# Performance work log

Hardware: AMD Instinct MI355X
Metric: run time of the kernel (lower is better)

The kernel has to match this reference:

```python
import jax, jax.numpy as jnp
import numpy as np

B, N, C, H, W = 2, 6, 64, 28, 50
D = 59  # len(arange(1.0, 60.0, 1.0))
BH, BW = 200, 200
BEV_X0, BEV_Y0 = -50.0, -50.0
RES_X, RES_Y = 0.5, 0.5  # (50-(-50))/200


def setup_inputs() -> dict:
    key = jax.random.key(0)
    k1, k2 = jax.random.split(key)
    features = jax.random.normal(k1, (B, N, C, H, W), dtype=jnp.float32)
    # depth distribution over D bins (softmax-normalized, as a depth net would emit)
    depth = jax.nn.softmax(jax.random.normal(k2, (B, N, D, H, W), dtype=jnp.float32), axis=2)
    # realistic pinhole intrinsics for a WxH feature map
    K = np.zeros((B, N, 3, 3), np.float32)
    K[..., 0, 0] = float(W)
    K[..., 1, 1] = float(W)
    K[..., 0, 2] = W / 2.0
    K[..., 1, 2] = H / 2.0
    K[..., 2, 2] = 1.0
    # cam-to-ego extrinsics: axis remap (z_cam->x_ego, x_cam->-y_ego, y_cam->-z_ego)
    # composed with a per-camera yaw, plus a small mounting translation
    R0 = np.array([[0, 0, 1], [-1, 0, 0], [0, -1, 0]], np.float32)
    E = np.zeros((B, N, 4, 4), np.float32)
    for n in range(N):
        yaw = 2.0 * np.pi * n / N
        Rz = np.array([[np.cos(yaw), -np.sin(yaw), 0.0],
                       [np.sin(yaw), np.cos(yaw), 0.0],
                       [0.0, 0.0, 1.0]], np.float32)
        E[:, n, :3, :3] = Rz @ R0
        E[:, n, 0, 3] = 1.5 * np.cos(yaw)
        E[:, n, 1, 3] = 1.5 * np.sin(yaw)
        E[:, n, 2, 3] = 1.6
    E[..., 3, 3] = 1.0
    return {
        "features": features,
        "depth": depth,
        "intrinsics": jnp.asarray(K),
        "extrinsics": jnp.asarray(E),
    }


def _frustum_ego(intrinsics, extrinsics):
    # pixel grid (H, W, 3) homogeneous coords
    xs = jnp.linspace(0.0, W - 1.0, W, dtype=jnp.float32)
    ys = jnp.linspace(0.0, H - 1.0, H, dtype=jnp.float32)
    yy, xx = jnp.meshgrid(ys, xs, indexing="ij")
    pix = jnp.stack([xx, yy, jnp.ones_like(xx)], axis=-1)  # (H, W, 3)
    depth_bins = jnp.arange(1.0, 60.0, 1.0, dtype=jnp.float32)  # (D,)
    frustum_cam = pix[None] * depth_bins[:, None, None, None]  # (D, H, W, 3)
    K_inv = jnp.linalg.inv(intrinsics)  # (B, N, 3, 3)
    cam = jnp.einsum("bnij,dhwj->bndhwi", K_inv, frustum_cam)  # (B, N, D, H, W, 3)
    R = extrinsics[..., :3, :3]
    t = extrinsics[..., :3, 3]
    ego = jnp.einsum("bnij,bndhwj->bndhwi", R, cam) + t[:, :, None, None, None, :]
    return ego


def reference(features, depth, intrinsics, extrinsics):
    ego = _frustum_ego(intrinsics, extrinsics)  # (B, N, D, H, W, 3)

    # lift: outer product of features (B,N,C,H,W) and depth (B,N,D,H,W)
    lifted = features[:, :, None] * depth[:, :, :, None]  # (B, N, D, C, H, W)
    lifted = lifted.transpose(0, 1, 2, 4, 5, 3).reshape(B, -1, C)  # b (n d h w) c

    fr = ego.reshape(B, -1, 3)  # b (n d h w) xyz
    x, y, z = fr[..., 0], fr[..., 1], fr[..., 2]
    # torch .long() truncates toward zero -> astype(int32) matches
    bx = ((x - BEV_X0) / RES_X).astype(jnp.int32)
    by = ((y - BEV_Y0) / RES_Y).astype(jnp.int32)
    valid = (bx >= 0) & (bx < BW) & (by >= 0) & (by < BH) & (z > 0)

    # flat scatter index with per-batch offset; invalid -> dummy segment (dropped)
    b_off = (jnp.arange(B, dtype=jnp.int32) * (BH * BW))[:, None]
    flat_idx = jnp.where(valid, b_off + by * BW + bx, B * BH * BW)
    seg = jax.ops.segment_sum(
        lifted.reshape(-1, C), flat_idx.reshape(-1), num_segments=B * BH * BW + 1
    )
    bev = seg[: B * BH * BW].reshape(B, BH, BW, C).transpose(0, 3, 1, 2)  # (B, C, BH, BW)
    return bev
```

## Files before the change

kernel.cpp:

```cpp
#include <hip/hip_runtime.h>
#include <hip/hip_bf16.h>

#define Bc 2
#define Nc 6
#define Cc 64
#define Hc 28
#define Wc 50
#define Dc 59
#define BHc 200
#define BWc 200

#define DSPLIT 2
#define DCHUNK 32
#define DWAVE 8

__global__ __launch_bounds__(256) void fp_scatter3(
    const float* __restrict__ feats,
    const float* __restrict__ depth,
    const float* __restrict__ Kmat,
    const float* __restrict__ Emat,
    float* __restrict__ acc)
{
    __shared__ __align__(16) float feat_lds[Hc][Cc];
    __shared__ __align__(16) float mdep[Hc][DCHUNK];

    int blk   = blockIdx.x;
    int dhalf = blk & 1;
    int pix   = blk >> 1;
    int w  = pix % Wc;
    int bn = pix / Wc;
    int b  = bn / Nc;
    int tid  = threadIdx.x;
    int lane = tid & 63;
    int wid  = tid >> 6;

    const size_t HW = (size_t)Hc * Wc;
    const float* fbase = feats + (size_t)bn * Cc * HW + w;
    const float* dbase = depth + (size_t)bn * Dc * HW + w;

    for (int h = wid; h < Hc; h += 4)
        feat_lds[h][lane] = fbase[(size_t)lane * HW + (size_t)h * Wc];

    const float* K = Kmat + (size_t)bn * 9;
    float k00 = K[0], k01 = K[1], k02 = K[2];
    float k10 = K[3], k11 = K[4], k12 = K[5];
    float k20 = K[6], k21 = K[7], k22 = K[8];

    float c00 = __fsub_rn(__fmul_rn(k11, k22), __fmul_rn(k12, k21));
    float c01 = __fsub_rn(__fmul_rn(k12, k20), __fmul_rn(k10, k22));
    float c02 = __fsub_rn(__fmul_rn(k10, k21), __fmul_rn(k11, k20));
    float det = __fadd_rn(__fadd_rn(__fmul_rn(k00, c00), __fmul_rn(k01, c01)),
                          __fmul_rn(k02, c02));
    float i00 = __fdiv_rn(c00, det);
    float i01 = __fdiv_rn(__fsub_rn(__fmul_rn(k02, k21), __fmul_rn(k01, k22)), det);
    float i02 = __fdiv_rn(__fsub_rn(__fmul_rn(k01, k12), __fmul_rn(k02, k11)), det);
    float i10 = __fdiv_rn(c01, det);
    float i11 = __fdiv_rn(__fsub_rn(__fmul_rn(k00, k22), __fmul_rn(k02, k20)), det);
    float i12 = __fdiv_rn(__fsub_rn(__fmul_rn(k02, k10), __fmul_rn(k00, k12)), det);
    float i20 = __fdiv_rn(c02, det);
    float i21 = __fdiv_rn(__fsub_rn(__fmul_rn(k01, k20), __fmul_rn(k00, k21)), det);
    float i22 = __fdiv_rn(__fsub_rn(__fmul_rn(k00, k11), __fmul_rn(k01, k10)), det);

    const float* E = Emat + (size_t)bn * 16;
    float r00 = E[0], r01 = E[1], r02 = E[2],  tx = E[3];
    float r10 = E[4], r11 = E[5], r12 = E[6],  ty = E[7];
    float r20 = E[8], r21 = E[9], r22 = E[10], tz = E[11];

    __syncthreads();

    float* accb = acc + (size_t)b * (BHc * BWc) * Cc;

    int h = lane;
    float xf = (float)w;
    float yf = (float)h;
    int ld0 = wid * DWAVE;

    float accv[DWAVE];
    int   prim[DWAVE];

#pragma unroll
    for (int k = 0; k < DWAVE; ++k) {
        accv[k] = 0.0f;
        prim[k] = -1;
        int ld = ld0 + k;
        int dg = dhalf * DCHUNK + ld;
        if (dg < Dc) {
            float db = (float)(dg + 1);
            float dep = 0.0f;
            if (h < Hc) dep = dbase[(size_t)dg * HW + (size_t)h * Wc];

            float px = __fmul_rn(xf, db);
            float py = __fmul_rn(yf, db);
            float pz = db;

            float cx = __fadd_rn(__fadd_rn(__fmul_rn(i00, px), __fmul_rn(i01, py)), __fmul_rn(i02, pz));
            float cy = __fadd_rn(__fadd_rn(__fmul_rn(i10, px), __fmul_rn(i11, py)), __fmul_rn(i12, pz));
            float cz = __fadd_rn(__fadd_rn(__fmul_rn(i20, px), __fmul_rn(i21, py)), __fmul_rn(i22, pz));

            float ex = __fadd_rn(__fadd_rn(__fadd_rn(__fmul_rn(r00, cx), __fmul_rn(r01, cy)), __fmul_rn(r02, cz)), tx);
            float ey = __fadd_rn(__fadd_rn(__fadd_rn(__fmul_rn(r10, cx), __fmul_rn(r11, cy)), __fmul_rn(r12, cz)), ty);
            float ez = __fadd_rn(__fadd_rn(__fadd_rn(__fmul_rn(r20, cx), __fmul_rn(r21, cy)), __fmul_rn(r22, cz)), tz);

            int bx = (int)(__fmul_rn(__fadd_rn(ex, 50.0f), 2.0f));
            int by = (int)(__fmul_rn(__fadd_rn(ey, 50.0f), 2.0f));

            bool valid = (h < Hc) & (bx >= 0) & (bx < BWc) & (by >= 0) & (by < BHc) & (ez > 0.0f);
            int binidx = by * BWc + bx;

            unsigned long long vm = __ballot(valid);
            float val = 0.0f;
            if (vm != 0ULL) {
                int first = __builtin_ctzll(vm);
                int pr = __shfl(binidx, first);
                unsigned long long match = __ballot(valid && (binidx == pr));
                unsigned long long rest  = vm & ~match;
                prim[k] = pr;
                val = (valid && (binidx == pr)) ? dep : 0.0f;

                while (rest) {
                    int hh2 = __builtin_ctzll(rest);
                    rest &= rest - 1;
                    int   bidx = __shfl(binidx, hh2);
                    float dv   = __shfl(dep, hh2);
                    atomicAdd(&accb[(size_t)bidx * Cc + lane],
                              __fmul_rn(feat_lds[hh2][lane], dv));
                }
            }
            if (h < Hc) {
                char* base = (char*)&mdep[h][0];
                *(float*)(base + (((ld << 2) ^ ((h & 7) << 4)))) = val;
            }
        }
    }

    int lb0 = ld0 >> 2;
#pragma unroll
    for (int hh = 0; hh < Hc; ++hh) {
        float f = feat_lds[hh][lane];
        const float4* rowp = (const float4*)&mdep[hh][0];
        float4 v0 = rowp[(lb0 + 0) ^ (hh & 7)];
        float4 v1 = rowp[(lb0 + 1) ^ (hh & 7)];
        accv[0] = __builtin_fmaf(f, v0.x, accv[0]);
        accv[1] = __builtin_fmaf(f, v0.y, accv[1]);
        accv[2] = __builtin_fmaf(f, v0.z, accv[2]);
        accv[3] = __builtin_fmaf(f, v0.w, accv[3]);
        accv[4] = __builtin_fmaf(f, v1.x, accv[4]);
        accv[5] = __builtin_fmaf(f, v1.y, accv[5]);
        accv[6] = __builtin_fmaf(f, v1.z, accv[6]);
        accv[7] = __builtin_fmaf(f, v1.w, accv[7]);
    }

#pragma unroll
    for (int k = 0; k < DWAVE; ++k) {
        if (prim[k] >= 0)
            atomicAdd(&accb[(size_t)prim[k] * Cc + lane], accv[k]);
    }
}

__global__ __launch_bounds__(256) void fp_transpose_kernel(
    const float* __restrict__ acc, float* __restrict__ out)
{
    __shared__ float tile[64][65];
    const int P = BHc * BWc;
    int b = blockIdx.y;
    int p0 = blockIdx.x * 64;
    int tx = threadIdx.x & 63;
    int ty = threadIdx.x >> 6;

    const float* src = acc + (size_t)b * P * Cc;
#pragma unroll
    for (int i = 0; i < 16; ++i) {
        int row = ty * 16 + i;
        tile[row][tx] = src[(size_t)(p0 + row) * Cc + tx];
    }
    __syncthreads();
    float* dst = out + (size_t)b * Cc * P;
#pragma unroll
    for (int i = 0; i < 16; ++i) {
        int c = ty * 16 + i;
        dst[(size_t)c * P + p0 + tx] = tile[tx][c];
    }
}

extern "C" void kernel_launch(void* const* d_in, const int* in_sizes, int n_in,
                              void* d_out, int out_size, void* d_ws, size_t ws_size,
                              hipStream_t stream) {
    const float* feats = (const float*)d_in[0];
    const float* depth = (const float*)d_in[1];
    const float* Kmat  = (const float*)d_in[2];
    const float* Emat  = (const float*)d_in[3];
    float* out = (float*)d_out;

    const size_t ACC_ELEMS = (size_t)Bc * BHc * BWc * Cc;
    const size_t ACC_BYTES = ACC_ELEMS * sizeof(float);
    float* acc = (float*)d_ws;

    hipMemsetAsync(acc, 0, ACC_BYTES, stream);

    const int NBLK = Bc * Nc * Wc * DSPLIT;
    fp_scatter3<<<NBLK, 256, 0, stream>>>(feats, depth, Kmat, Emat, acc);

    fp_transpose_kernel<<<dim3((BHc * BWc) / 64, Bc), 256, 0, stream>>>(acc, out);
}
```

Measured before the change: 118.6 us.

## Pre-transpose features and depth for coalesced loads, split depth into four chunks

Adds a pre-pass kernel that transposes features to (bn,h,w,c) and depth to (bn,d,w,h) in workspace, so the scatter kernel reads them with contiguous, coalesced loads instead of strided ones. The scatter kernel now splits the depth range into four chunks of 16 (four bins per wave), which doubles the block count and shrinks the per-thread accumulator arrays. The cost is an extra kernel launch and a full extra read and write of both inputs, plus features being reloaded by twice as many blocks.

```diff
diff --git a/kernel.cpp b/kernel.cpp
--- a/kernel.cpp
+++ b/kernel.cpp
@@ -10,23 +10,75 @@
 #define BHc 200
 #define BWc 200
 
-#define DSPLIT 2
-#define DCHUNK 32
-#define DWAVE 8
-
-__global__ __launch_bounds__(256) void fp_scatter3(
+#define DSPLIT 4
+#define DCHUNK 16
+#define DWAVE 4
+
+#define HWc (Hc * Wc)
+#define NT1 (Bc * Nc * 22)
+#define NT2 (Bc * Nc * Dc)
+
+__global__ __launch_bounds__(256) void fp_pretrans(
     const float* __restrict__ feats,
     const float* __restrict__ depth,
+    float* __restrict__ Fp,
+    float* __restrict__ Dpp)
+{
+    __shared__ float t[64][65];
+    __shared__ float t2[Hc][Wc + 1];
+
+    int bid = blockIdx.x;
+    int tid = threadIdx.x;
+
+    if (bid < NT1) {
+        int bn  = bid / 22;
+        int hw0 = (bid % 22) * 64;
+        int tx = tid & 63;
+        int ty = tid >> 6;
+        const float* src = feats + (size_t)bn * Cc * HWc;
+        float* dst = Fp + (size_t)bn * HWc * Cc;
+#pragma unroll
+        for (int i = 0; i < 16; ++i) {
+            int c = ty * 16 + i;
+            int hw = hw0 + tx;
+            t[c][tx] = (hw < HWc) ? src[(size_t)c * HWc + hw] : 0.0f;
+        }
+        __syncthreads();
+#pragma unroll
+        for (int i = 0; i < 16; ++i) {
+            int j = ty * 16 + i;
+            if (hw0 + j < HWc)
+                dst[(size_t)(hw0 + j) * Cc + tx] = t[tx][j];
+        }
+    } else {
+        int bid2 = bid - NT1;
+        int bn = bid2 / Dc;
+        int d  = bid2 % Dc;
+        const float* sp = depth + ((size_t)bn * Dc + d) * HWc;
+        float* dp = Dpp + ((size_t)bn * Dc + d) * HWc;
+        for (int idx = tid; idx < HWc; idx += 256)
+            t2[idx / Wc][idx % Wc] = sp[idx];
+        __syncthreads();
+        for (int idx = tid; idx < HWc; idx += 256) {
+            int w = idx / Hc, h = idx % Hc;
+            dp[idx] = t2[h][w];
+        }
+    }
+}
+
+__global__ __launch_bounds__(256) void fp_scatter4(
+    const float* __restrict__ Fp,
+    const float* __restrict__ Dpp,
     const float* __restrict__ Kmat,
     const float* __restrict__ Emat,
     float* __restrict__ acc)
 {
     __shared__ __align__(16) float feat_lds[Hc][Cc];
-    __shared__ __align__(16) float mdep[Hc][DCHUNK];
-
-    int blk   = blockIdx.x;
-    int dhalf = blk & 1;
-    int pix   = blk >> 1;
+    __shared__ __align__(16) float mdep[Hc][20];
+
+    int bid = blockIdx.x;
+    int dq  = bid & (DSPLIT - 1);
+    int pix = bid >> 2;
     int w  = pix % Wc;
     int bn = pix / Wc;
     int b  = bn / Nc;
@@ -34,12 +86,9 @@
     int lane = tid & 63;
     int wid  = tid >> 6;
 
-    const size_t HW = (size_t)Hc * Wc;
-    const float* fbase = feats + (size_t)bn * Cc * HW + w;
-    const float* dbase = depth + (size_t)bn * Dc * HW + w;
-
-    for (int h = wid; h < Hc; h += 4)
-        feat_lds[h][lane] = fbase[(size_t)lane * HW + (size_t)h * Wc];
+    const float* fbase = Fp + ((size_t)bn * Hc * Wc + w) * Cc;
+    for (int hh = wid; hh < Hc; hh += 4)
+        feat_lds[hh][lane] = fbase[(size_t)hh * Wc * Cc + lane];
 
     const float* K = Kmat + (size_t)bn * 9;
     float k00 = K[0], k01 = K[1], k02 = K[2];
@@ -83,11 +132,12 @@
         accv[k] = 0.0f;
         prim[k] = -1;
         int ld = ld0 + k;
-        int dg = dhalf * DCHUNK + ld;
+        int dg = dq * DCHUNK + ld;
         if (dg < Dc) {
             float db = (float)(dg + 1);
             float dep = 0.0f;
-            if (h < Hc) dep = dbase[(size_t)dg * HW + (size_t)h * Wc];
+            if (h < Hc)
+                dep = Dpp[(((size_t)bn * Dc + dg) * Wc + w) * Hc + h];
 
             float px = __fmul_rn(xf, db);
             float py = __fmul_rn(yf, db);
@@ -126,28 +176,20 @@
                               __fmul_rn(feat_lds[hh2][lane], dv));
                 }
             }
-            if (h < Hc) {
-                char* base = (char*)&mdep[h][0];
-                *(float*)(base + (((ld << 2) ^ ((h & 7) << 4)))) = val;
-            }
-        }
-    }
-
-    int lb0 = ld0 >> 2;
+            if (h < Hc)
+                mdep[h][ld ^ ((h & 3) << 2)] = val;
+        }
+    }
+
 #pragma unroll
     for (int hh = 0; hh < Hc; ++hh) {
         float f = feat_lds[hh][lane];
         const float4* rowp = (const float4*)&mdep[hh][0];
-        float4 v0 = rowp[(lb0 + 0) ^ (hh & 7)];
-        float4 v1 = rowp[(lb0 + 1) ^ (hh & 7)];
+        float4 v0 = rowp[wid ^ (hh & 3)];
         accv[0] = __builtin_fmaf(f, v0.x, accv[0]);
         accv[1] = __builtin_fmaf(f, v0.y, accv[1]);
         accv[2] = __builtin_fmaf(f, v0.z, accv[2]);
         accv[3] = __builtin_fmaf(f, v0.w, accv[3]);
-        accv[4] = __builtin_fmaf(f, v1.x, accv[4]);
-        accv[5] = __builtin_fmaf(f, v1.y, accv[5]);
-        accv[6] = __builtin_fmaf(f, v1.z, accv[6]);
-        accv[7] = __builtin_fmaf(f, v1.w, accv[7]);
     }
 
 #pragma unroll
@@ -193,12 +235,20 @@
 
     const size_t ACC_ELEMS = (size_t)Bc * BHc * BWc * Cc;
     const size_t ACC_BYTES = ACC_ELEMS * sizeof(float);
+    const size_t F_ELEMS = (size_t)Bc * Nc * Hc * Wc * Cc;
+    const size_t D_ELEMS = (size_t)Bc * Nc * Dc * Hc * Wc;
+
     float* acc = (float*)d_ws;
+    float* Fp  = acc + ACC_ELEMS;
+    float* Dpp = Fp + F_ELEMS;
+    (void)D_ELEMS;
 
     hipMemsetAsync(acc, 0, ACC_BYTES, stream);
 
+    fp_pretrans<<<NT1 + NT2, 256, 0, stream>>>(feats, depth, Fp, Dpp);
+
     const int NBLK = Bc * Nc * Wc * DSPLIT;
-    fp_scatter3<<<NBLK, 256, 0, stream>>>(feats, depth, Kmat, Emat, acc);
+    fp_scatter4<<<NBLK, 256, 0, stream>>>(Fp, Dpp, Kmat, Emat, acc);
 
     fp_transpose_kernel<<<dim3((BHc * BWc) / 64, Bc), 256, 0, stream>>>(acc, out);
 }
```

Result: faster. 111.9 us (-5.7%).

## Merge depth halves into 512-thread blocks, broadcast depths via readlane

Applied to the files above, without the earlier changes.

The scatter kernel now gives each (camera, column) one 512-thread block with eight waves. Each wave takes interleaved depth bins, which removes the two-way depth split and halves the feature loads into LDS. The LDS depth buffer and its swizzled float4 reads are replaced by per-wave register values broadcast with readlane. Block indices are permuted, likely to spread work across chiplets, and the hipMemset is replaced by a custom float4 zeroing kernel. In exchange there are fewer, larger blocks, which lowers the number of blocks that can overlap atomic latency, and each wave carries more readlane instructions.

```diff
diff --git a/kernel.cpp b/kernel.cpp
--- a/kernel.cpp
+++ b/kernel.cpp
@@ -10,11 +10,25 @@
 #define BHc 200
 #define BWc 200
 
-#define DSPLIT 2
-#define DCHUNK 32
+#define HWc (Hc * Wc)
+#define NWAVES 8
 #define DWAVE 8
-
-__global__ __launch_bounds__(256) void fp_scatter3(
+#define NZ 640
+#define ACC_ELEMS ((size_t)Bc * BHc * BWc * Cc)
+
+__global__ __launch_bounds__(256) void fp_zero(float* __restrict__ acc)
+{
+    const size_t NF4 = ACC_ELEMS / 4;
+    float4* a4 = (float4*)acc;
+    size_t base = (size_t)blockIdx.x * 2048;
+#pragma unroll
+    for (int it = 0; it < 8; ++it) {
+        size_t i = base + (size_t)it * 256 + threadIdx.x;
+        if (i < NF4) a4[i] = make_float4(0.f, 0.f, 0.f, 0.f);
+    }
+}
+
+__global__ __launch_bounds__(512) void fp_scatter6(
     const float* __restrict__ feats,
     const float* __restrict__ depth,
     const float* __restrict__ Kmat,
@@ -22,24 +36,22 @@
     float* __restrict__ acc)
 {
     __shared__ __align__(16) float feat_lds[Hc][Cc];
-    __shared__ __align__(16) float mdep[Hc][DCHUNK];
-
-    int blk   = blockIdx.x;
-    int dhalf = blk & 1;
-    int pix   = blk >> 1;
-    int w  = pix % Wc;
-    int bn = pix / Wc;
-    int b  = bn / Nc;
+
+    int bid = blockIdx.x;
+    int L   = (bid & 7) * 75 + (bid >> 3);
+    int w   = L % Wc;
+    int bn  = L / Wc;
+    int b   = bn / Nc;
     int tid  = threadIdx.x;
     int lane = tid & 63;
     int wid  = tid >> 6;
 
-    const size_t HW = (size_t)Hc * Wc;
+    const size_t HW = (size_t)HWc;
     const float* fbase = feats + (size_t)bn * Cc * HW + w;
-    const float* dbase = depth + (size_t)bn * Dc * HW + w;
-
-    for (int h = wid; h < Hc; h += 4)
-        feat_lds[h][lane] = fbase[(size_t)lane * HW + (size_t)h * Wc];
+    const float* dcol  = depth + (size_t)bn * Dc * HW + w;
+
+    for (int hh = wid; hh < Hc; hh += NWAVES)
+        feat_lds[hh][lane] = fbase[(size_t)lane * HW + (size_t)hh * Wc];
 
     const float* K = Kmat + (size_t)bn * 9;
     float k00 = K[0], k01 = K[1], k02 = K[2];
@@ -73,21 +85,22 @@
     int h = lane;
     float xf = (float)w;
     float yf = (float)h;
-    int ld0 = wid * DWAVE;
 
     float accv[DWAVE];
+    float mval[DWAVE];
     int   prim[DWAVE];
 
 #pragma unroll
     for (int k = 0; k < DWAVE; ++k) {
         accv[k] = 0.0f;
+        mval[k] = 0.0f;
         prim[k] = -1;
-        int ld = ld0 + k;
-        int dg = dhalf * DCHUNK + ld;
+        int dg = wid + NWAVES * k;
         if (dg < Dc) {
             float db = (float)(dg + 1);
             float dep = 0.0f;
-            if (h < Hc) dep = dbase[(size_t)dg * HW + (size_t)h * Wc];
+            if (h < Hc)
+                dep = dcol[(size_t)dg * HW + (size_t)h * Wc];
 
             float px = __fmul_rn(xf, db);
             float py = __fmul_rn(yf, db);
@@ -108,14 +121,13 @@
             int binidx = by * BWc + bx;
 
             unsigned long long vm = __ballot(valid);
-            float val = 0.0f;
             if (vm != 0ULL) {
                 int first = __builtin_ctzll(vm);
                 int pr = __shfl(binidx, first);
                 unsigned long long match = __ballot(valid && (binidx == pr));
                 unsigned long long rest  = vm & ~match;
                 prim[k] = pr;
-                val = (valid && (binidx == pr)) ? dep : 0.0f;
+                mval[k] = (valid && (binidx == pr)) ? dep : 0.0f;
 
                 while (rest) {
                     int hh2 = __builtin_ctzll(rest);
@@ -126,28 +138,18 @@
                               __fmul_rn(feat_lds[hh2][lane], dv));
                 }
             }
-            if (h < Hc) {
-                char* base = (char*)&mdep[h][0];
-                *(float*)(base + (((ld << 2) ^ ((h & 7) << 4)))) = val;
-            }
         }
     }
 
-    int lb0 = ld0 >> 2;
 #pragma unroll
     for (int hh = 0; hh < Hc; ++hh) {
         float f = feat_lds[hh][lane];
-        const float4* rowp = (const float4*)&mdep[hh][0];
-        float4 v0 = rowp[(lb0 + 0) ^ (hh & 7)];
-        float4 v1 = rowp[(lb0 + 1) ^ (hh & 7)];
-        accv[0] = __builtin_fmaf(f, v0.x, accv[0]);
-        accv[1] = __builtin_fmaf(f, v0.y, accv[1]);
-        accv[2] = __builtin_fmaf(f, v0.z, accv[2]);
-        accv[3] = __builtin_fmaf(f, v0.w, accv[3]);
-        accv[4] = __builtin_fmaf(f, v1.x, accv[4]);
-        accv[5] = __builtin_fmaf(f, v1.y, accv[5]);
-        accv[6] = __builtin_fmaf(f, v1.z, accv[6]);
-        accv[7] = __builtin_fmaf(f, v1.w, accv[7]);
+#pragma unroll
+        for (int k = 0; k < DWAVE; ++k) {
+            float dk = __int_as_float(
+                __builtin_amdgcn_readlane(__float_as_int(mval[k]), hh));
+            accv[k] = __builtin_fmaf(f, dk, accv[k]);
+        }
     }
 
 #pragma unroll
@@ -191,14 +193,11 @@
     const float* Emat  = (const float*)d_in[3];
     float* out = (float*)d_out;
 
-    const size_t ACC_ELEMS = (size_t)Bc * BHc * BWc * Cc;
-    const size_t ACC_BYTES = ACC_ELEMS * sizeof(float);
     float* acc = (float*)d_ws;
 
-    hipMemsetAsync(acc, 0, ACC_BYTES, stream);
-
-    const int NBLK = Bc * Nc * Wc * DSPLIT;
-    fp_scatter3<<<NBLK, 256, 0, stream>>>(feats, depth, Kmat, Emat, acc);
+    fp_zero<<<NZ, 256, 0, stream>>>(acc);
+
+    fp_scatter6<<<600, 512, 0, stream>>>(feats, depth, Kmat, Emat, acc);
 
     fp_transpose_kernel<<<dim3((BHc * BWc) / 64, Bc), 256, 0, stream>>>(acc, out);
 }
```

Measured after the change: 97.09 us. 1.22x faster.
